# Optimization experiments

Measured on AMD Instinct MI355X. Metric: run time of the kernel, lower is better.

Reference implementation:

```python
import jax, jax.numpy as jnp
import numpy as np

BN, C, P = 1024, 32, 7          # patches, feat channels, patch size
G, MAX_DISP, DS = 8, 160, 1     # groups, max disparity, downsample rate
D = MAX_DISP // DS              # disparity bins = hypergraph nodes N
K, TH = 3, 16                   # kNN k, spatial threshold
W = P + MAX_DISP                # right strip width
NEG = -1e9


def setup_inputs() -> dict:
    key = jax.random.key(0)
    ks = jax.random.split(key, 7)
    left_feat = jax.random.normal(ks[0], (BN, C, P, P), jnp.float32)
    right_feat = jax.random.normal(ks[1], (BN, C, P, W), jnp.float32)
    start_left = jax.random.randint(ks[2], (BN,), 0, MAX_DISP + 1)
    f1_w = jax.random.normal(ks[3], (G, G), jnp.float32) / np.sqrt(G)
    f1_b = jax.random.normal(ks[4], (G,), jnp.float32) * 0.01
    conv_w = jax.random.normal(ks[5], (1, G, 3), jnp.float32) / np.sqrt(3 * G)
    conv_b = jax.random.normal(ks[6], (1,), jnp.float32) * 0.01
    return dict(left_feat=left_feat, right_feat=right_feat, start_left=start_left,
                f1_w=f1_w, f1_b=f1_b, conv_w=conv_w, conv_b=conv_b)


def _square_distance(src, dst):
    d = -2.0 * jnp.einsum('bnc,bmc->bnm', src, dst)
    return d + jnp.sum(src ** 2, -1)[:, :, None] + jnp.sum(dst ** 2, -1)[:, None, :]


def _mean_agg(X, path):
    # X' = path @ X, then mean-normalize rows; 1/0 -> 0 as in torch (isinf -> 0)
    out = jnp.einsum('brc,bcf->brf', path, X)
    s = jnp.sum(path, axis=2, keepdims=True)
    return jnp.where(s > 0, out / jnp.where(s > 0, s, 1.0), 0.0)


def _hypconv(x, H, f1_w, f1_b):
    # Linear -> LeakyReLU -> Dropout(eval: identity) -> v2e -> e2v
    h = jax.nn.leaky_relu(x @ f1_w.T + f1_b, 0.01)
    E = _mean_agg(h, jnp.swapaxes(H, 1, 2))
    return _mean_agg(E, H)


def _forward(left_feat, right_feat, f1_w, f1_b, conv_w, conv_b, start_left):
    bn = left_feat.shape[0]
    d_vals = jnp.arange(D) * DS
    # group-wise correlation cost volume: right window at column start_left - d
    cols = start_left[:, None, None] - d_vals[None, :, None] + jnp.arange(P)[None, None, :]  # [bn,D,P]
    valid = jnp.all((cols >= 0) & (cols < W), axis=2).astype(left_feat.dtype)                # [bn,D]
    cols_c = jnp.clip(cols, 0, W - 1).reshape(bn, 1, 1, D * P)
    r = jnp.take_along_axis(right_feat, cols_c, axis=3).reshape(bn, C, P, D, P)
    lg = left_feat.reshape(bn, G, C // G, P, P)
    rg = r.reshape(bn, G, C // G, P, D, P)
    vol = jnp.einsum('bgcyx,bgcydx->bgd', lg, rg) / (C // G * P * P)
    vol = vol * valid[:, None, :]                          # [bn,G,D]
    mask = jnp.sum(vol, axis=1, keepdims=True) == 0        # [bn,1,D]

    feature = jnp.swapaxes(vol, 1, 2)                      # [bn,D,G] nodes x feats
    _, idx = jax.lax.top_k(-_square_distance(feature, feature), K)  # k smallest dists, [bn,D,K]
    pos = jnp.arange(D)[None, :, None]
    near = jnp.abs(idx - pos) < TH
    row_pos = jnp.where(near, idx, D)                      # far neighbors -> dummy row D
    row_neg = jnp.where(near, D, idx)
    b_i = jnp.arange(bn)[:, None, None]
    c_i = jnp.arange(D)[None, :, None]
    hg_pos = jnp.zeros((bn, D + 1, D), feature.dtype).at[b_i, row_pos, c_i].set(1.0)[:, :D, :]
    hg_neg = jnp.zeros((bn, D + 1, D), feature.dtype).at[b_i, row_neg, c_i].set(1.0)[:, :D, :]

    # HGNNPN: note the original uses hgconv1 for BOTH branches (hgconv2 is dead)
    x1 = _hypconv(feature, hg_pos, f1_w, f1_b)
    x2 = _hypconv(feature, hg_neg, f1_w, f1_b)
    feat = feature + 0.1 * x1 - 0.1 * x2

    cv = jnp.swapaxes(feat, 1, 2)                          # [bn,G,D]
    agg = jax.lax.conv_general_dilated(cv, conv_w, (1,), [(1, 1)],
                                       dimension_numbers=('NCH', 'OIH', 'NCH'))
    agg = agg + conv_b[None, :, None]
    agg = jnp.where(mask, NEG, agg)
    prob = jax.nn.softmax(agg, axis=2).reshape(bn, -1)
    return jnp.sum(prob * d_vals.astype(prob.dtype), axis=1) * DS


def reference(left_feat, right_feat, start_left, f1_w, f1_b, conv_w, conv_b):
    return _forward(left_feat, right_feat, f1_w, f1_b, conv_w, conv_b, start_left)
```

## Files before the change

kernel.cpp:

```cpp
#include <hip/hip_runtime.h>
#include <math.h>

#define TBN 1024
#define TC  32
#define TP  7
#define TG  8
#define TD  160
#define TW  167
#define TK  3
#define TTH 16
#define CPG 4
#define NEGV -1e9f

typedef float f4 __attribute__((ext_vector_type(4)));

__global__ __launch_bounds__(256, 4)
void patchmix_kernel(const float* __restrict__ left,
                     const float* __restrict__ right,
                     const int*   __restrict__ start_left,
                     const float* __restrict__ f1w,
                     const float* __restrict__ f1b,
                     const float* __restrict__ convw,
                     const float* __restrict__ convb,
                     float* __restrict__ out)
{
    __shared__ float s_left[TC * TP * TP];
    __shared__ __align__(16) float s_feat[TD][TG];
    __shared__ float s_h[TD * 9];
    __shared__ float s_accP[TD * 9];
    __shared__ float s_accN[TD * 9];
    __shared__ float s_norm[TD];
    __shared__ float s_agg[TD];
    __shared__ float s_f1w[TG * TG];
    __shared__ float s_f1b[TG];
    __shared__ float s_cw[TG * 3];
    __shared__ float s_cb;
    __shared__ int   s_idx[TD][TK];
    __shared__ int   s_near[TD][TK];
    __shared__ int   s_degP[TD];
    __shared__ int   s_degN[TD];

    const int bn = blockIdx.x;
    const int t  = threadIdx.x;
    const int start = start_left[bn];

    {
        const float* lsrc = left + bn * (TC * TP * TP);
        for (int i = t; i < TC * TP * TP; i += 256) s_left[i] = lsrc[i];
        if (t < 64)        s_f1w[t]      = f1w[t];
        else if (t < 72)   s_f1b[t - 64] = f1b[t - 64];
        else if (t < 96)   s_cw[t - 72]  = convw[t - 72];
        else if (t == 96)  s_cb          = convb[0];
    }
    __syncthreads();

    for (int task = t; task < 320; task += 256) {
        const int g  = task / 40;
        const int dq = task - g * 40;
        const int d0 = dq * 4;
        float a0 = 0.f, a1 = 0.f, a2 = 0.f, a3 = 0.f;
        if (d0 <= start) {
            const int col0 = start - d0 - 3;
            const float* rp = right + ((bn * TC + g * CPG) * TP) * TW + col0;
            const float* lp = s_left + g * CPG * TP * TP;
            for (int cy = 0; cy < CPG * TP; ++cy) {
                float r0, r1, r2, r3, r4, r5, r6, r7, r8, r9;
                if (col0 >= 0) {
                    r0 = rp[0]; r1 = rp[1]; r2 = rp[2]; r3 = rp[3]; r4 = rp[4];
                    r5 = rp[5]; r6 = rp[6]; r7 = rp[7]; r8 = rp[8]; r9 = rp[9];
                } else {
                    r0 = (col0 + 0 >= 0) ? rp[0] : 0.f;
                    r1 = (col0 + 1 >= 0) ? rp[1] : 0.f;
                    r2 = (col0 + 2 >= 0) ? rp[2] : 0.f;
                    r3 = rp[3]; r4 = rp[4]; r5 = rp[5];
                    r6 = rp[6]; r7 = rp[7]; r8 = rp[8]; r9 = rp[9];
                }
                const float l0 = lp[0], l1 = lp[1], l2 = lp[2], l3 = lp[3],
                            l4 = lp[4], l5 = lp[5], l6 = lp[6];
#define FMAROW(acc, rA, rB, rC, rD, rE, rF, rG) \
                acc = fmaf(l0, rA, acc); acc = fmaf(l1, rB, acc); \
                acc = fmaf(l2, rC, acc); acc = fmaf(l3, rD, acc); \
                acc = fmaf(l4, rE, acc); acc = fmaf(l5, rF, acc); \
                acc = fmaf(l6, rG, acc);
                FMAROW(a0, r3, r4, r5, r6, r7, r8, r9)
                FMAROW(a1, r2, r3, r4, r5, r6, r7, r8)
                FMAROW(a2, r1, r2, r3, r4, r5, r6, r7)
                FMAROW(a3, r0, r1, r2, r3, r4, r5, r6)
#undef FMAROW
                rp += TW;
                lp += TP;
            }
        }
        s_feat[d0 + 0][g] = (d0 + 0 <= start) ? a0 / 196.0f : 0.f;
        s_feat[d0 + 1][g] = (d0 + 1 <= start) ? a1 / 196.0f : 0.f;
        s_feat[d0 + 2][g] = (d0 + 2 <= start) ? a2 / 196.0f : 0.f;
        s_feat[d0 + 3][g] = (d0 + 3 <= start) ? a3 / 196.0f : 0.f;
    }
    __syncthreads();

    if (t < TD) {
        float s = 0.f;
#pragma unroll
        for (int g = 0; g < TG; ++g) { float v = s_feat[t][g]; s = fmaf(v, v, s); }
        s_norm[t] = s;
    }
    __syncthreads();

    if (t < TD) {
        const f4 fa = ((const f4*)s_feat[t])[0];
        const f4 fb = ((const f4*)s_feat[t])[1];
        const float ni = s_norm[t];
        float v0 = 3e38f, v1 = 3e38f, v2 = 3e38f;
        int   i0 = -1,    i1 = -1,    i2 = -1;
        for (int j = 0; j < TD; ++j) {
            const f4 ga = ((const f4*)s_feat[j])[0];
            const f4 gb = ((const f4*)s_feat[j])[1];
            float dot = fa.x * ga.x + fa.y * ga.y + fa.z * ga.z + fa.w * ga.w
                      + fb.x * gb.x + fb.y * gb.y + fb.z * gb.z + fb.w * gb.w;
            float dist = ni + s_norm[j] - 2.f * dot;
            if (dist < v2) {
                v2 = dist; i2 = j;
                if (v2 < v1) {
                    float tv = v1; v1 = v2; v2 = tv; int ti = i1; i1 = i2; i2 = ti;
                    if (v1 < v0) {
                        tv = v0; v0 = v1; v1 = tv; ti = i0; i0 = i1; i1 = ti;
                    }
                }
            }
        }
        s_idx[t][0] = i0; s_idx[t][1] = i1; s_idx[t][2] = i2;
        int dk0 = i0 - t, dk1 = i1 - t, dk2 = i2 - t;
        s_near[t][0] = (dk0 < TTH && dk0 > -TTH);
        s_near[t][1] = (dk1 < TTH && dk1 > -TTH);
        s_near[t][2] = (dk2 < TTH && dk2 > -TTH);
    } else {
        for (int i = t - TD; i < TD * 9; i += 96) { s_accP[i] = 0.f; s_accN[i] = 0.f; }
        for (int i = t - TD; i < TD;     i += 96) { s_degP[i] = 0;   s_degN[i] = 0;   }
    }
    __syncthreads();

    for (int task = t; task < TD * TG; task += 256) {
        const int d = task >> 3, go = task & 7;
        float s = s_f1b[go];
#pragma unroll
        for (int gi = 0; gi < TG; ++gi) s = fmaf(s_feat[d][gi], s_f1w[go * TG + gi], s);
        s_h[d * 9 + go] = (s >= 0.f) ? s : 0.01f * s;
    }
    __syncthreads();

    if (t < TD) {
        const int jj[3] = { s_idx[t][0], s_idx[t][1], s_idx[t][2] };
        const int nr[3] = { s_near[t][0], s_near[t][1], s_near[t][2] };
        float ep[TG] = {0, 0, 0, 0, 0, 0, 0, 0};
        float en[TG] = {0, 0, 0, 0, 0, 0, 0, 0};
        int cp = 0, cn = 0;
#pragma unroll
        for (int k = 0; k < TK; ++k) {
            const float* hp = &s_h[jj[k] * 9];
            if (nr[k]) { cp++;
#pragma unroll
                for (int g = 0; g < TG; ++g) ep[g] += hp[g];
            } else { cn++;
#pragma unroll
                for (int g = 0; g < TG; ++g) en[g] += hp[g];
            }
        }
        if (cp) {
#pragma unroll
            for (int g = 0; g < TG; ++g) ep[g] /= (float)cp;
        }
        if (cn) {
#pragma unroll
            for (int g = 0; g < TG; ++g) en[g] /= (float)cn;
        }
#pragma unroll
        for (int k = 0; k < TK; ++k) {
            if (nr[k]) {
                atomicAdd(&s_degP[jj[k]], 1);
#pragma unroll
                for (int g = 0; g < TG; ++g) atomicAdd(&s_accP[jj[k] * 9 + g], ep[g]);
            } else {
                atomicAdd(&s_degN[jj[k]], 1);
#pragma unroll
                for (int g = 0; g < TG; ++g) atomicAdd(&s_accN[jj[k] * 9 + g], en[g]);
            }
        }
    }
    __syncthreads();

    if (t < TD) {
        const int dp = s_degP[t], dn = s_degN[t];
#pragma unroll
        for (int g = 0; g < TG; ++g) {
            float x1 = dp ? s_accP[t * 9 + g] / (float)dp : 0.f;
            float x2 = dn ? s_accN[t * 9 + g] / (float)dn : 0.f;
            s_accP[t * 9 + g] = s_feat[t][g] + 0.1f * x1 - 0.1f * x2;
        }
    }
    __syncthreads();

    if (t < TD) {
        float msum = 0.f;
#pragma unroll
        for (int g = 0; g < TG; ++g) msum += s_feat[t][g];
        float a = s_cb;
#pragma unroll
        for (int kw = 0; kw < 3; ++kw) {
            const int dd = t + kw - 1;
            if (dd >= 0 && dd < TD) {
#pragma unroll
                for (int g = 0; g < TG; ++g)
                    a = fmaf(s_accP[dd * 9 + g], s_cw[g * 3 + kw], a);
            }
        }
        s_agg[t] = (msum == 0.f) ? NEGV : a;
    }
    __syncthreads();

    if (t < 64) {
        float m = -3e38f;
        for (int d = t; d < TD; d += 64) m = fmaxf(m, s_agg[d]);
#pragma unroll
        for (int off = 32; off; off >>= 1) m = fmaxf(m, __shfl_xor(m, off, 64));
        float se = 0.f, sd = 0.f;
        for (int d = t; d < TD; d += 64) {
            float e = expf(s_agg[d] - m);
            se += e;
            sd = fmaf(e, (float)d, sd);
        }
#pragma unroll
        for (int off = 32; off; off >>= 1) {
            se += __shfl_xor(se, off, 64);
            sd += __shfl_xor(sd, off, 64);
        }
        if (t == 0) out[bn] = sd / se;
    }
}

extern "C" void kernel_launch(void* const* d_in, const int* in_sizes, int n_in,
                              void* d_out, int out_size, void* d_ws, size_t ws_size,
                              hipStream_t stream) {
    const float* left   = (const float*)d_in[0];
    const float* right  = (const float*)d_in[1];
    const int*   start  = (const int*)d_in[2];
    const float* f1w    = (const float*)d_in[3];
    const float* f1b    = (const float*)d_in[4];
    const float* convw  = (const float*)d_in[5];
    const float* convb  = (const float*)d_in[6];
    float* out = (float*)d_out;
    patchmix_kernel<<<TBN, 256, 0, stream>>>(left, right, start, f1w, f1b,
                                             convw, convb, out);
}
```

Measured before the change: 294.6 us.

## Remap cost-volume work to 5 disparities per thread with padded vectorized left loads

The correlation stage now assigns exactly one task per thread (8 groups x 32 lanes, 5 disparities each) instead of 320 tasks over 256 threads, removing the tail iteration. Left patch rows are padded to 8 floats in shared memory so they can be read as float4 vectors. Right rows are double-buffered in registers across a 2-row unrolled loop, and the boundary handling becomes clamped offsets instead of a branch. The padded left buffer aliases the accumulator arrays to keep LDS use down, at the cost of more registers per thread and an extra reset of the shared pool.

```diff
diff --git a/kernel.cpp b/kernel.cpp
--- a/kernel.cpp
+++ b/kernel.cpp
@@ -24,11 +24,9 @@
                      const float* __restrict__ convb,
                      float* __restrict__ out)
 {
-    __shared__ float s_left[TC * TP * TP];
+    __shared__ __align__(16) float s_pool[2880];
     __shared__ __align__(16) float s_feat[TD][TG];
     __shared__ float s_h[TD * 9];
-    __shared__ float s_accP[TD * 9];
-    __shared__ float s_accN[TD * 9];
     __shared__ float s_norm[TD];
     __shared__ float s_agg[TD];
     __shared__ float s_f1w[TG * TG];
@@ -40,13 +38,21 @@
     __shared__ int   s_degP[TD];
     __shared__ int   s_degN[TD];
 
+    float* const s_lp   = s_pool;
+    float* const s_accP = s_pool;
+    float* const s_accN = s_pool + 1440;
+
     const int bn = blockIdx.x;
     const int t  = threadIdx.x;
     const int start = start_left[bn];
 
     {
         const float* lsrc = left + bn * (TC * TP * TP);
-        for (int i = t; i < TC * TP * TP; i += 256) s_left[i] = lsrc[i];
+        for (int i = t; i < TC * TP * TP; i += 256) {
+            const int cy = i / 7;
+            const int x  = i - cy * 7;
+            s_lp[cy * 8 + x] = lsrc[i];
+        }
         if (t < 64)        s_f1w[t]      = f1w[t];
         else if (t < 72)   s_f1b[t - 64] = f1b[t - 64];
         else if (t < 96)   s_cw[t - 72]  = convw[t - 72];
@@ -54,47 +60,63 @@
     }
     __syncthreads();
 
-    for (int task = t; task < 320; task += 256) {
-        const int g  = task / 40;
-        const int dq = task - g * 40;
-        const int d0 = dq * 4;
-        float a0 = 0.f, a1 = 0.f, a2 = 0.f, a3 = 0.f;
+    {
+        const int g  = t >> 5;
+        const int d0 = (t & 31) * 5;
+        float a0 = 0.f, a1 = 0.f, a2 = 0.f, a3 = 0.f, a4 = 0.f;
         if (d0 <= start) {
-            const int col0 = start - d0 - 3;
+            const int col0 = start - d0 - 4;
             const float* rp = right + ((bn * TC + g * CPG) * TP) * TW + col0;
-            const float* lp = s_left + g * CPG * TP * TP;
-            for (int cy = 0; cy < CPG * TP; ++cy) {
-                float r0, r1, r2, r3, r4, r5, r6, r7, r8, r9;
-                if (col0 >= 0) {
-                    r0 = rp[0]; r1 = rp[1]; r2 = rp[2]; r3 = rp[3]; r4 = rp[4];
-                    r5 = rp[5]; r6 = rp[6]; r7 = rp[7]; r8 = rp[8]; r9 = rp[9];
-                } else {
-                    r0 = (col0 + 0 >= 0) ? rp[0] : 0.f;
-                    r1 = (col0 + 1 >= 0) ? rp[1] : 0.f;
-                    r2 = (col0 + 2 >= 0) ? rp[2] : 0.f;
-                    r3 = rp[3]; r4 = rp[4]; r5 = rp[5];
-                    r6 = rp[6]; r7 = rp[7]; r8 = rp[8]; r9 = rp[9];
+            const float* lq = s_lp + g * (CPG * TP) * 8;
+            const int o0 = (col0 >=  0) ? 0 : 4;
+            const int o1 = (col0 >= -1) ? 1 : 4;
+            const int o2 = (col0 >= -2) ? 2 : 4;
+            const int o3 = (col0 >= -3) ? 3 : 4;
+            float w0,w1,w2,w3,w4,w5,w6,w7,w8,w9,w10;
+            float x0,x1,x2,x3,x4,x5,x6,x7,x8,x9,x10;
+#define LOADW(b0,b1,b2,b3,b4,b5,b6,b7,b8,b9,b10,p) \
+            b0=(p)[o0]; b1=(p)[o1]; b2=(p)[o2]; b3=(p)[o3]; b4=(p)[4]; \
+            b5=(p)[5]; b6=(p)[6]; b7=(p)[7]; b8=(p)[8]; b9=(p)[9]; b10=(p)[10];
+#define FMA5(la,lb,r0,r1,r2,r3,r4,r5,r6,r7,r8,r9,r10) \
+            a0=fmaf(la.x,r4,a0);  a0=fmaf(la.y,r5,a0);  a0=fmaf(la.z,r6,a0); \
+            a0=fmaf(la.w,r7,a0);  a0=fmaf(lb.x,r8,a0);  a0=fmaf(lb.y,r9,a0); \
+            a0=fmaf(lb.z,r10,a0); \
+            a1=fmaf(la.x,r3,a1);  a1=fmaf(la.y,r4,a1);  a1=fmaf(la.z,r5,a1); \
+            a1=fmaf(la.w,r6,a1);  a1=fmaf(lb.x,r7,a1);  a1=fmaf(lb.y,r8,a1); \
+            a1=fmaf(lb.z,r9,a1); \
+            a2=fmaf(la.x,r2,a2);  a2=fmaf(la.y,r3,a2);  a2=fmaf(la.z,r4,a2); \
+            a2=fmaf(la.w,r5,a2);  a2=fmaf(lb.x,r6,a2);  a2=fmaf(lb.y,r7,a2); \
+            a2=fmaf(lb.z,r8,a2); \
+            a3=fmaf(la.x,r1,a3);  a3=fmaf(la.y,r2,a3);  a3=fmaf(la.z,r3,a3); \
+            a3=fmaf(la.w,r4,a3);  a3=fmaf(lb.x,r5,a3);  a3=fmaf(lb.y,r6,a3); \
+            a3=fmaf(lb.z,r7,a3); \
+            a4=fmaf(la.x,r0,a4);  a4=fmaf(la.y,r1,a4);  a4=fmaf(la.z,r2,a4); \
+            a4=fmaf(la.w,r3,a4);  a4=fmaf(lb.x,r4,a4);  a4=fmaf(lb.y,r5,a4); \
+            a4=fmaf(lb.z,r6,a4);
+
+            LOADW(w0,w1,w2,w3,w4,w5,w6,w7,w8,w9,w10, rp)
+            for (int h = 0; h < 14; ++h) {
+                const f4 la0 = *(const f4*)(lq);
+                const f4 lb0 = *(const f4*)(lq + 4);
+                const f4 la1 = *(const f4*)(lq + 8);
+                const f4 lb1 = *(const f4*)(lq + 12);
+                LOADW(x0,x1,x2,x3,x4,x5,x6,x7,x8,x9,x10, rp + TW)
+                FMA5(la0, lb0, w0,w1,w2,w3,w4,w5,w6,w7,w8,w9,w10)
+                rp += 2 * TW;
+                if (h < 13) {
+                    LOADW(w0,w1,w2,w3,w4,w5,w6,w7,w8,w9,w10, rp)
                 }
-                const float l0 = lp[0], l1 = lp[1], l2 = lp[2], l3 = lp[3],
-                            l4 = lp[4], l5 = lp[5], l6 = lp[6];
-#define FMAROW(acc, rA, rB, rC, rD, rE, rF, rG) \
-                acc = fmaf(l0, rA, acc); acc = fmaf(l1, rB, acc); \
-                acc = fmaf(l2, rC, acc); acc = fmaf(l3, rD, acc); \
-                acc = fmaf(l4, rE, acc); acc = fmaf(l5, rF, acc); \
-                acc = fmaf(l6, rG, acc);
-                FMAROW(a0, r3, r4, r5, r6, r7, r8, r9)
-                FMAROW(a1, r2, r3, r4, r5, r6, r7, r8)
-                FMAROW(a2, r1, r2, r3, r4, r5, r6, r7)
-                FMAROW(a3, r0, r1, r2, r3, r4, r5, r6)
-#undef FMAROW
-                rp += TW;
-                lp += TP;
-            }
+                FMA5(la1, lb1, x0,x1,x2,x3,x4,x5,x6,x7,x8,x9,x10)
+                lq += 16;
+            }
+#undef LOADW
+#undef FMA5
         }
         s_feat[d0 + 0][g] = (d0 + 0 <= start) ? a0 / 196.0f : 0.f;
         s_feat[d0 + 1][g] = (d0 + 1 <= start) ? a1 / 196.0f : 0.f;
         s_feat[d0 + 2][g] = (d0 + 2 <= start) ? a2 / 196.0f : 0.f;
         s_feat[d0 + 3][g] = (d0 + 3 <= start) ? a3 / 196.0f : 0.f;
+        s_feat[d0 + 4][g] = (d0 + 4 <= start) ? a4 / 196.0f : 0.f;
     }
     __syncthreads();
 
@@ -134,8 +156,8 @@
         s_near[t][1] = (dk1 < TTH && dk1 > -TTH);
         s_near[t][2] = (dk2 < TTH && dk2 > -TTH);
     } else {
-        for (int i = t - TD; i < TD * 9; i += 96) { s_accP[i] = 0.f; s_accN[i] = 0.f; }
-        for (int i = t - TD; i < TD;     i += 96) { s_degP[i] = 0;   s_degN[i] = 0;   }
+        for (int i = t - TD; i < 2880; i += 96) s_pool[i] = 0.f;
+        for (int i = t - TD; i < TD;   i += 96) { s_degP[i] = 0; s_degN[i] = 0; }
     }
     __syncthreads();
 
```

Result: no change. 289.2 us (-1.8%).
